# Optimization experiments

Hardware: AMD Instinct MI355X
Metric: run time of the kernel (lower is better)

Reference implementation:

```python
import jax, jax.numpy as jnp
import numpy as np
import math

# tcnn HashGrid config (instant-ngp defaults, Smoothstep interpolation)
N_LEVELS = 16
F_PER_LEVEL = 2
LOG2_T = 19
T = 1 << LOG2_T            # hashmap size per level
BASE_RES = 16
PER_LEVEL_SCALE = 2.0
PRIMES = (1, 2654435761)   # tcnn spatial hash primes for 2D
IN_DIM = 2

# 4 corner offsets of the 2D cell, tcnn ordering (dim0 fastest)
_OFFSETS = jnp.array([[0, 0], [1, 0], [0, 1], [1, 1]], dtype=jnp.int32)  # [4,2]


def setup_inputs() -> dict:
    key = jax.random.key(0)
    k1, k2 = jax.random.split(key)
    # atlas coords in [-1, 1] as the wrapper expects (it maps to [0,1])
    x = jax.random.uniform(k1, (64, 64, 128, IN_DIM), jnp.float32, -1.0, 1.0)
    # tcnn initializes hash tables uniform in [-1e-4, 1e-4]
    table = jax.random.uniform(k2, (N_LEVELS, T, F_PER_LEVEL), jnp.float32, -1e-4, 1e-4)
    return {"x": x, "table": table}


def _encode(x01, table):
    # x01: [N, 2] in [0, 1]; table: [L, T, F]
    outs = []
    for l in range(N_LEVELS):
        # grid_scale = exp2(level * log2(per_level_scale)) * base_resolution - 1
        scale = (PER_LEVEL_SCALE ** l) * BASE_RES - 1.0
        res = int(math.ceil(scale)) + 1
        pos = x01 * jnp.float32(scale) + 0.5
        pg = jnp.floor(pos)
        frac = pos - pg                       # [N,2]
        pg = pg.astype(jnp.int32)
        # Smoothstep interpolation weights
        w = frac * frac * (3.0 - 2.0 * frac)  # [N,2]
        corners = pg[:, None, :] + _OFFSETS[None]                     # [N,4,2]
        cw = jnp.where(_OFFSETS[None].astype(bool),
                       w[:, None, :], 1.0 - w[:, None, :]).prod(-1)   # [N,4]
        if res * res <= T:
            # dense (non-hashed) level: row-major index, wrapped like tcnn
            idx = (corners[..., 0] + corners[..., 1] * res) % (res * res)
        else:
            cu = corners.astype(jnp.uint32)
            h = (cu[..., 0] * jnp.uint32(PRIMES[0])) ^ (cu[..., 1] * jnp.uint32(PRIMES[1]))
            idx = (h & jnp.uint32(T - 1)).astype(jnp.int32)
        feats = table[l][idx]                                         # [N,4,F]
        outs.append((cw[..., None] * feats).sum(axis=1))              # [N,F]
    return jnp.concatenate(outs, axis=-1)                             # [N, L*F]


def reference(x, table):
    Nv, Nr, Nm, C = x.shape
    x01 = x.reshape(-1, C) * 0.5 + 0.5
    enc = _encode(x01, table)
    return enc.reshape(Nv, Nr, Nm, -1)
```

## Files before the change

kernel.cpp:

```cpp
#include <hip/hip_runtime.h>
#include <stdint.h>


#define HG_LEVELS 16
#define HG_T (1u << 19)
#define HG_PRIME1 2654435761u

typedef float vfloat2 __attribute__((ext_vector_type(2)));
typedef float vfloat4 __attribute__((ext_vector_type(4)));

__global__ __launch_bounds__(256, 4) void hashgrid_encode5_kernel(
    const float* __restrict__ x,
    const float* __restrict__ table,
    float* __restrict__ out,
    int npts)
{
    int i = blockIdx.x * blockDim.x + threadIdx.x;
    if (i >= npts) i = npts - 1;

    vfloat2 xi = __builtin_nontemporal_load((const vfloat2*)(x + 2 * (size_t)i));
    float x0 = xi.x * 0.5f + 0.5f;
    float x1 = xi.y * 0.5f + 0.5f;

    float acc[2 * HG_LEVELS];

#pragma unroll
    for (int l = 0; l < HG_LEVELS; ++l) {
        const int res = 16 << l;
        const float scale = (float)res - 1.0f;
        float p0 = x0 * scale + 0.5f;
        float p1 = x1 * scale + 0.5f;
        float g0 = floorf(p0);
        float g1 = floorf(p1);
        float fr0 = p0 - g0;
        float fr1 = p1 - g1;
        uint32_t c0 = (uint32_t)(int)g0;
        uint32_t c1 = (uint32_t)(int)g1;
        float w0 = fr0 * fr0 * (3.0f - 2.0f * fr0);
        float w1 = fr1 * fr1 * (3.0f - 2.0f * fr1);

        uint32_t i00, i10, i01, i11;
        if (l <= 5) {
            const uint32_t mask = (uint32_t)res * (uint32_t)res - 1u;
            uint32_t b0 = c1 * (uint32_t)res;
            uint32_t b1 = (c1 + 1u) * (uint32_t)res;
            i00 = (c0 + b0) & mask;
            i10 = (c0 + 1u + b0) & mask;
            i01 = (c0 + b1) & mask;
            i11 = (c0 + 1u + b1) & mask;
        } else {
            uint32_t h0 = c1 * HG_PRIME1;
            uint32_t h1 = (c1 + 1u) * HG_PRIME1;
            i00 = (c0 ^ h0) & (HG_T - 1u);
            i10 = ((c0 + 1u) ^ h0) & (HG_T - 1u);
            i01 = (c0 ^ h1) & (HG_T - 1u);
            i11 = ((c0 + 1u) ^ h1) & (HG_T - 1u);
        }

        const float2* tl = (const float2*)(table + (size_t)l * (size_t)HG_T * 2u);
        float2 f00 = tl[i00];
        float2 f10 = tl[i10];
        float2 f01 = tl[i01];
        float2 f11 = tl[i11];

        float w00 = (1.0f - w0) * (1.0f - w1);
        float w10 = w0 * (1.0f - w1);
        float w01 = (1.0f - w0) * w1;
        float w11 = w0 * w1;

        acc[2 * l + 0] = w00 * f00.x + w10 * f10.x + w01 * f01.x + w11 * f11.x;
        acc[2 * l + 1] = w00 * f00.y + w10 * f10.y + w01 * f01.y + w11 * f11.y;

        if (l >= 5 && l < HG_LEVELS - 1) __syncthreads();
    }

    float* o = out + (size_t)i * (2 * HG_LEVELS);
#pragma unroll
    for (int j = 0; j < 8; ++j) {
        vfloat4 v = { acc[4 * j + 0], acc[4 * j + 1],
                      acc[4 * j + 2], acc[4 * j + 3] };
        __builtin_nontemporal_store(v, (vfloat4*)(o + 4 * j));
    }
}

extern "C" void kernel_launch(void* const* d_in, const int* in_sizes, int n_in,
                              void* d_out, int out_size, void* d_ws, size_t ws_size,
                              hipStream_t stream) {
    const float* x = (const float*)d_in[0];
    const float* table = (const float*)d_in[1];
    float* out = (float*)d_out;

    int npts = in_sizes[0] / 2;
    int block = 256;
    int grid = (npts + block - 1) / block;
    hashgrid_encode5_kernel<<<grid, block, 0, stream>>>(x, table, out, npts);
}
```

Baseline: 325.9 us.

## Split encoding into per-level gather kernel pinned to XCDs plus transpose pass

Replaces the single per-point kernel with a two-kernel scheme. The first kernel assigns each block one level and a chunk of points, mapping the level to blockIdx&7 so each XCD's L2 serves only two levels' tables, and processes two points per thread. It writes level-major results to workspace, and a second kernel transposes them into the point-major output. This targets L2 locality for the random table gathers at the cost of an extra round trip through workspace and a second launch; a fallback kernel is used when workspace is too small.

```diff
diff --git a/kernel.cpp b/kernel.cpp
--- a/kernel.cpp
+++ b/kernel.cpp
@@ -9,78 +9,170 @@
 typedef float vfloat2 __attribute__((ext_vector_type(2)));
 typedef float vfloat4 __attribute__((ext_vector_type(4)));
 
-__global__ __launch_bounds__(256, 4) void hashgrid_encode5_kernel(
+__global__ __launch_bounds__(256) void hg_gather_kernel(
     const float* __restrict__ x,
     const float* __restrict__ table,
+    float* __restrict__ scratch,
+    int npts, int CH)
+{
+    int bid = blockIdx.x;
+    int xcd = bid & 7;
+    int slot = bid >> 3;
+    int level = (slot < CH) ? xcd : xcd + 8;
+    int chunk = (slot < CH) ? slot : slot - CH;
+
+    int p0 = chunk * 512 + 2 * (int)threadIdx.x;
+    if (p0 + 1 >= npts) p0 = npts - 2;
+
+    vfloat4 xp = __builtin_nontemporal_load((const vfloat4*)(x + 2 * (size_t)p0));
+    float a0 = xp.x * 0.5f + 0.5f;
+    float a1 = xp.y * 0.5f + 0.5f;
+    float b0 = xp.z * 0.5f + 0.5f;
+    float b1 = xp.w * 0.5f + 0.5f;
+
+    const int res = 16 << level;
+    const float scale = (float)res - 1.0f;
+    const bool dense = (level <= 5);
+    const uint32_t dmask = (uint32_t)res * (uint32_t)res - 1u;
+
+    float pA0 = a0 * scale + 0.5f, pA1 = a1 * scale + 0.5f;
+    float gA0 = floorf(pA0), gA1 = floorf(pA1);
+    float fA0 = pA0 - gA0, fA1 = pA1 - gA1;
+    uint32_t cA0 = (uint32_t)(int)gA0, cA1 = (uint32_t)(int)gA1;
+    float wA0 = fA0 * fA0 * (3.0f - 2.0f * fA0);
+    float wA1 = fA1 * fA1 * (3.0f - 2.0f * fA1);
+    float pB0 = b0 * scale + 0.5f, pB1 = b1 * scale + 0.5f;
+    float gB0 = floorf(pB0), gB1 = floorf(pB1);
+    float fB0 = pB0 - gB0, fB1 = pB1 - gB1;
+    uint32_t cB0 = (uint32_t)(int)gB0, cB1 = (uint32_t)(int)gB1;
+    float wB0 = fB0 * fB0 * (3.0f - 2.0f * fB0);
+    float wB1 = fB1 * fB1 * (3.0f - 2.0f * fB1);
+
+    uint32_t iA[4], iB[4];
+    if (dense) {
+        uint32_t bA0 = cA1 * (uint32_t)res, bA1 = (cA1 + 1u) * (uint32_t)res;
+        iA[0] = (cA0 + bA0) & dmask;  iA[1] = (cA0 + 1u + bA0) & dmask;
+        iA[2] = (cA0 + bA1) & dmask;  iA[3] = (cA0 + 1u + bA1) & dmask;
+        uint32_t bB0 = cB1 * (uint32_t)res, bB1 = (cB1 + 1u) * (uint32_t)res;
+        iB[0] = (cB0 + bB0) & dmask;  iB[1] = (cB0 + 1u + bB0) & dmask;
+        iB[2] = (cB0 + bB1) & dmask;  iB[3] = (cB0 + 1u + bB1) & dmask;
+    } else {
+        uint32_t hA0 = cA1 * HG_PRIME1, hA1 = (cA1 + 1u) * HG_PRIME1;
+        iA[0] = (cA0 ^ hA0) & (HG_T - 1u);  iA[1] = ((cA0 + 1u) ^ hA0) & (HG_T - 1u);
+        iA[2] = (cA0 ^ hA1) & (HG_T - 1u);  iA[3] = ((cA0 + 1u) ^ hA1) & (HG_T - 1u);
+        uint32_t hB0 = cB1 * HG_PRIME1, hB1 = (cB1 + 1u) * HG_PRIME1;
+        iB[0] = (cB0 ^ hB0) & (HG_T - 1u);  iB[1] = ((cB0 + 1u) ^ hB0) & (HG_T - 1u);
+        iB[2] = (cB0 ^ hB1) & (HG_T - 1u);  iB[3] = ((cB0 + 1u) ^ hB1) & (HG_T - 1u);
+    }
+
+    const float2* tl = (const float2*)(table + (size_t)level * (size_t)HG_T * 2u);
+    float2 fAv[4], fBv[4];
+#pragma unroll
+    for (int c = 0; c < 4; ++c) fAv[c] = tl[iA[c]];
+#pragma unroll
+    for (int c = 0; c < 4; ++c) fBv[c] = tl[iB[c]];
+
+    float wwA[4] = { (1.0f - wA0) * (1.0f - wA1), wA0 * (1.0f - wA1),
+                     (1.0f - wA0) * wA1,          wA0 * wA1 };
+    float wwB[4] = { (1.0f - wB0) * (1.0f - wB1), wB0 * (1.0f - wB1),
+                     (1.0f - wB0) * wB1,          wB0 * wB1 };
+
+    float sAx = 0.f, sAy = 0.f, sBx = 0.f, sBy = 0.f;
+#pragma unroll
+    for (int c = 0; c < 4; ++c) {
+        sAx += wwA[c] * fAv[c].x;  sAy += wwA[c] * fAv[c].y;
+        sBx += wwB[c] * fBv[c].x;  sBy += wwB[c] * fBv[c].y;
+    }
+
+    vfloat4 v = { sAx, sAy, sBx, sBy };
+    __builtin_nontemporal_store(
+        v, (vfloat4*)(scratch + ((size_t)level * (size_t)npts + (size_t)p0) * 2u));
+}
+
+__global__ __launch_bounds__(256) void hg_transpose_kernel(
+    const float* __restrict__ scratch,
     float* __restrict__ out,
     int npts)
 {
-    int i = blockIdx.x * blockDim.x + threadIdx.x;
-    if (i >= npts) i = npts - 1;
+    int p0 = blockIdx.x * 512 + 2 * (int)threadIdx.x;
+    if (p0 + 1 >= npts) p0 = npts - 2;
 
-    vfloat2 xi = __builtin_nontemporal_load((const vfloat2*)(x + 2 * (size_t)i));
-    float x0 = xi.x * 0.5f + 0.5f;
-    float x1 = xi.y * 0.5f + 0.5f;
+    float* o0 = out + (size_t)p0 * 32u;
+    float* o1 = o0 + 32u;
 
-    float acc[2 * HG_LEVELS];
+#pragma unroll
+    for (int j = 0; j < 8; ++j) {
+        vfloat4 a = __builtin_nontemporal_load(
+            (const vfloat4*)(scratch + ((size_t)(2 * j) * (size_t)npts + (size_t)p0) * 2u));
+        vfloat4 b = __builtin_nontemporal_load(
+            (const vfloat4*)(scratch + ((size_t)(2 * j + 1) * (size_t)npts + (size_t)p0) * 2u));
+        vfloat4 r0 = { a.x, a.y, b.x, b.y };
+        vfloat4 r1 = { a.z, a.w, b.z, b.w };
+        *(vfloat4*)(o0 + 4 * j) = r0;
+        *(vfloat4*)(o1 + 4 * j) = r1;
+    }
+}
 
+__global__ __launch_bounds__(256) void hg_fallback_kernel(
+    const float4* __restrict__ x, const float* __restrict__ table,
+    float* __restrict__ out, int npairs)
+{
+    int t = blockIdx.x * blockDim.x + threadIdx.x;
+    if (t >= npairs) t = npairs - 1;
+    float4 xp = x[t];
+    float a0 = xp.x * 0.5f + 0.5f, a1 = xp.y * 0.5f + 0.5f;
+    float b0 = xp.z * 0.5f + 0.5f, b1 = xp.w * 0.5f + 0.5f;
+    float accA[32], accB[32];
 #pragma unroll
     for (int l = 0; l < HG_LEVELS; ++l) {
         const int res = 16 << l;
         const float scale = (float)res - 1.0f;
-        float p0 = x0 * scale + 0.5f;
-        float p1 = x1 * scale + 0.5f;
-        float g0 = floorf(p0);
-        float g1 = floorf(p1);
-        float fr0 = p0 - g0;
-        float fr1 = p1 - g1;
-        uint32_t c0 = (uint32_t)(int)g0;
-        uint32_t c1 = (uint32_t)(int)g1;
-        float w0 = fr0 * fr0 * (3.0f - 2.0f * fr0);
-        float w1 = fr1 * fr1 * (3.0f - 2.0f * fr1);
-
-        uint32_t i00, i10, i01, i11;
+        float pA0 = a0 * scale + 0.5f, pA1 = a1 * scale + 0.5f;
+        float pB0 = b0 * scale + 0.5f, pB1 = b1 * scale + 0.5f;
+        float gA0 = floorf(pA0), gA1 = floorf(pA1), gB0 = floorf(pB0), gB1 = floorf(pB1);
+        float fA0 = pA0 - gA0, fA1 = pA1 - gA1, fB0 = pB0 - gB0, fB1 = pB1 - gB1;
+        uint32_t cA0 = (uint32_t)(int)gA0, cA1 = (uint32_t)(int)gA1;
+        uint32_t cB0 = (uint32_t)(int)gB0, cB1 = (uint32_t)(int)gB1;
+        float wA0 = fA0 * fA0 * (3.0f - 2.0f * fA0), wA1 = fA1 * fA1 * (3.0f - 2.0f * fA1);
+        float wB0 = fB0 * fB0 * (3.0f - 2.0f * fB0), wB1 = fB1 * fB1 * (3.0f - 2.0f * fB1);
+        uint32_t iA[4], iB[4];
         if (l <= 5) {
-            const uint32_t mask = (uint32_t)res * (uint32_t)res - 1u;
-            uint32_t b0 = c1 * (uint32_t)res;
-            uint32_t b1 = (c1 + 1u) * (uint32_t)res;
-            i00 = (c0 + b0) & mask;
-            i10 = (c0 + 1u + b0) & mask;
-            i01 = (c0 + b1) & mask;
-            i11 = (c0 + 1u + b1) & mask;
+            uint32_t mask = (uint32_t)res * (uint32_t)res - 1u;
+            uint32_t bA0 = cA1 * (uint32_t)res, bA1 = (cA1 + 1u) * (uint32_t)res;
+            uint32_t bB0 = cB1 * (uint32_t)res, bB1 = (cB1 + 1u) * (uint32_t)res;
+            iA[0]=(cA0+bA0)&mask; iA[1]=(cA0+1u+bA0)&mask; iA[2]=(cA0+bA1)&mask; iA[3]=(cA0+1u+bA1)&mask;
+            iB[0]=(cB0+bB0)&mask; iB[1]=(cB0+1u+bB0)&mask; iB[2]=(cB0+bB1)&mask; iB[3]=(cB0+1u+bB1)&mask;
         } else {
-            uint32_t h0 = c1 * HG_PRIME1;
-            uint32_t h1 = (c1 + 1u) * HG_PRIME1;
-            i00 = (c0 ^ h0) & (HG_T - 1u);
-            i10 = ((c0 + 1u) ^ h0) & (HG_T - 1u);
-            i01 = (c0 ^ h1) & (HG_T - 1u);
-            i11 = ((c0 + 1u) ^ h1) & (HG_T - 1u);
+            uint32_t hA0 = cA1*HG_PRIME1, hA1 = (cA1+1u)*HG_PRIME1;
+            uint32_t hB0 = cB1*HG_PRIME1, hB1 = (cB1+1u)*HG_PRIME1;
+            iA[0]=(cA0^hA0)&(HG_T-1u); iA[1]=((cA0+1u)^hA0)&(HG_T-1u);
+            iA[2]=(cA0^hA1)&(HG_T-1u); iA[3]=((cA0+1u)^hA1)&(HG_T-1u);
+            iB[0]=(cB0^hB0)&(HG_T-1u); iB[1]=((cB0+1u)^hB0)&(HG_T-1u);
+            iB[2]=(cB0^hB1)&(HG_T-1u); iB[3]=((cB0+1u)^hB1)&(HG_T-1u);
         }
-
         const float2* tl = (const float2*)(table + (size_t)l * (size_t)HG_T * 2u);
-        float2 f00 = tl[i00];
-        float2 f10 = tl[i10];
-        float2 f01 = tl[i01];
-        float2 f11 = tl[i11];
-
-        float w00 = (1.0f - w0) * (1.0f - w1);
-        float w10 = w0 * (1.0f - w1);
-        float w01 = (1.0f - w0) * w1;
-        float w11 = w0 * w1;
-
-        acc[2 * l + 0] = w00 * f00.x + w10 * f10.x + w01 * f01.x + w11 * f11.x;
-        acc[2 * l + 1] = w00 * f00.y + w10 * f10.y + w01 * f01.y + w11 * f11.y;
-
+        float2 fa[4], fb[4];
+#pragma unroll
+        for (int c = 0; c < 4; ++c) fa[c] = tl[iA[c]];
+#pragma unroll
+        for (int c = 0; c < 4; ++c) fb[c] = tl[iB[c]];
+        float wwA[4] = {(1.f-wA0)*(1.f-wA1), wA0*(1.f-wA1), (1.f-wA0)*wA1, wA0*wA1};
+        float wwB[4] = {(1.f-wB0)*(1.f-wB1), wB0*(1.f-wB1), (1.f-wB0)*wB1, wB0*wB1};
+        float sAx=0.f,sAy=0.f,sBx=0.f,sBy=0.f;
+#pragma unroll
+        for (int c = 0; c < 4; ++c) {
+            sAx += wwA[c]*fa[c].x; sAy += wwA[c]*fa[c].y;
+            sBx += wwB[c]*fb[c].x; sBy += wwB[c]*fb[c].y;
+        }
+        accA[2*l]=sAx; accA[2*l+1]=sAy; accB[2*l]=sBx; accB[2*l+1]=sBy;
         if (l >= 5 && l < HG_LEVELS - 1) __syncthreads();
     }
-
-    float* o = out + (size_t)i * (2 * HG_LEVELS);
+    float4* oA = (float4*)(out + (size_t)(2*t+0)*32u);
+    float4* oB = (float4*)(out + (size_t)(2*t+1)*32u);
 #pragma unroll
-    for (int j = 0; j < 8; ++j) {
-        vfloat4 v = { acc[4 * j + 0], acc[4 * j + 1],
-                      acc[4 * j + 2], acc[4 * j + 3] };
-        __builtin_nontemporal_store(v, (vfloat4*)(o + 4 * j));
-    }
+    for (int j = 0; j < 8; ++j) oA[j] = make_float4(accA[4*j],accA[4*j+1],accA[4*j+2],accA[4*j+3]);
+#pragma unroll
+    for (int j = 0; j < 8; ++j) oB[j] = make_float4(accB[4*j],accB[4*j+1],accB[4*j+2],accB[4*j+3]);
 }
 
 extern "C" void kernel_launch(void* const* d_in, const int* in_sizes, int n_in,
@@ -91,7 +183,17 @@
     float* out = (float*)d_out;
 
     int npts = in_sizes[0] / 2;
-    int block = 256;
-    int grid = (npts + block - 1) / block;
-    hashgrid_encode5_kernel<<<grid, block, 0, stream>>>(x, table, out, npts);
+    size_t need = (size_t)HG_LEVELS * (size_t)npts * 2u * sizeof(float);
+
+    if (ws_size >= need && d_ws != nullptr) {
+        float* scratch = (float*)d_ws;
+        int CH = (npts + 511) / 512;
+        int grid1 = 16 * CH;
+        hg_gather_kernel<<<grid1, 256, 0, stream>>>(x, table, scratch, npts, CH);
+        hg_transpose_kernel<<<CH, 256, 0, stream>>>(scratch, out, npts);
+    } else {
+        int npairs = npts / 2;
+        int grid = (npairs + 255) / 256;
+        hg_fallback_kernel<<<grid, 256, 0, stream>>>((const float4*)x, table, out, npairs);
+    }
 }
```

Measured after the change: 263.6 us. 1.24x faster.
